# Kernel optimization log

Hardware: AMD Instinct MI355X
Metric: run time of the kernel (lower is better)

## Reference

```python
import jax, jax.numpy as jnp
import numpy as np

NUM_HEADS = 16
INPUT_SIZE = 1024
KEY_SIZE = 64
VALUE_SIZE = 64
LN_EPS = 1e-5


def setup_inputs() -> dict:
    key = jax.random.key(0)
    ks = jax.random.split(key, 11)
    B, S, D = 2, 2048, INPUT_SIZE
    Hk = NUM_HEADS * KEY_SIZE
    Hv = NUM_HEADS * VALUE_SIZE
    s = 0.02
    return {
        "queries": jax.random.normal(ks[0], (B, S, D), dtype=jnp.float32),
        "Wq": jax.random.normal(ks[1], (D, Hk), dtype=jnp.float32) * s,
        "bq": jnp.zeros((Hk,), dtype=jnp.float32),
        "Wk": jax.random.normal(ks[2], (D, Hk), dtype=jnp.float32) * s,
        "bk": jnp.zeros((Hk,), dtype=jnp.float32),
        "Wv": jax.random.normal(ks[3], (D, Hv), dtype=jnp.float32) * s,
        "bv": jnp.zeros((Hv,), dtype=jnp.float32),
        "Wo": jax.random.normal(ks[4], (Hv, D), dtype=jnp.float32) * s,
        "bo": jnp.zeros((D,), dtype=jnp.float32),
        "ln_gamma": jnp.ones((D,), dtype=jnp.float32),
        "ln_beta": jnp.zeros((D,), dtype=jnp.float32),
    }


def reference(queries, Wq, bq, Wk, bk, Wv, bv, Wo, bo, ln_gamma, ln_beta):
    B, S, D = queries.shape
    H, dk, dv = NUM_HEADS, KEY_SIZE, VALUE_SIZE
    residual = queries
    # projections -> [B, S, H, d]
    q = (queries @ Wq + bq).reshape(B, S, H, dk)
    k = (queries @ Wk + bk).reshape(B, S, H, dk)
    v = (queries @ Wv + bv).reshape(B, S, H, dv)
    # scaled dot-product attention per head
    scores = jnp.einsum("bqhd,bkhd->bhqk", q, k) / jnp.sqrt(jnp.float32(dk))
    attn = jax.nn.softmax(scores, axis=-1)
    out = jnp.einsum("bhqk,bkhd->bqhd", attn, v).reshape(B, S, H * dv)
    # out projection + residual + layernorm (dropout=0 / eval)
    res = out @ Wo + bo + residual
    mu = jnp.mean(res, axis=-1, keepdims=True)
    var = jnp.var(res, axis=-1, keepdims=True)
    return (res - mu) / jnp.sqrt(var + LN_EPS) * ln_gamma + ln_beta
```

## Files before the change

kernel.cpp:

```cpp
#include <hip/hip_runtime.h>
#include <hip/hip_bf16.h>
#include <math.h>

#define D 1024
#define NH 16
#define DK 64
#define LN_EPS 1e-5f
typedef __hip_bfloat16 bf16;
typedef __attribute__((ext_vector_type(8))) short bf16x8;
typedef __attribute__((ext_vector_type(4))) short short4v;
typedef __attribute__((ext_vector_type(4))) float f32x4;
typedef __attribute__((ext_vector_type(2))) unsigned int uint2v;

__device__ inline float tofloat(bf16 x) { return __bfloat162float(x); }
__device__ inline float tofs(short s) {
    bf16 b; __builtin_memcpy(&b, &s, 2);
    return __bfloat162float(b);
}
__device__ inline unsigned int pk2(float a, float b) {
    float2 f2; f2.x = a; f2.y = b;
    __hip_bfloat162 h = __float22bfloat162_rn(f2);
    unsigned int u; __builtin_memcpy(&u, &h, 4);
    return u;
}
__device__ inline short4v pk4(float a, float b, float c, float d) {
    uint2v u; u[0] = pk2(a, b); u[1] = pk2(c, d);
    short4v s; __builtin_memcpy(&s, &u, 8);
    return s;
}
__device__ inline bf16x8 pk8(const float* f) {
    uint2v a, b;
    a[0] = pk2(f[0], f[1]); a[1] = pk2(f[2], f[3]);
    b[0] = pk2(f[4], f[5]); b[1] = pk2(f[6], f[7]);
    bf16x8 o;
    short4v s0, s1;
    __builtin_memcpy(&s0, &a, 8); __builtin_memcpy(&s1, &b, 8);
#pragma unroll
    for (int i = 0; i < 4; ++i) { o[i] = s0[i]; o[4 + i] = s1[i]; }
    return o;
}

__device__ inline int wave_isf32(const unsigned short* __restrict__ Xu) {
    unsigned short u = Xu[threadIdx.x & 63];
    unsigned long long m = __ballot(((u >> 7) & 0xFF) >= 0x90);
    return __popcll(m) > 2;
}

__global__ void prep_kernel(const void* X, const void* Wq, const void* Wk, const void* Wv,
                            const void* Wo, const void* bq, const void* bk, const void* bv,
                            const void* bo, const void* g, const void* be,
                            bf16* __restrict__ Xb, bf16* __restrict__ Wqkvt, bf16* __restrict__ Wot,
                            bf16* __restrict__ bqkv, bf16* __restrict__ bob,
                            bf16* __restrict__ gb, bf16* __restrict__ beb) {
    __shared__ float tile[64][65];
    const int isf32 = wave_isf32((const unsigned short*)X);
    const int bid = blockIdx.x;
    const int tid = threadIdx.x;
    if (bid < 2048) {
        int e0 = bid * 2048 + tid * 8;
        bf16x8 outv;
        if (isf32) {
            float4 v0 = ((const float4*)X)[e0 / 4];
            float4 v1 = ((const float4*)X)[e0 / 4 + 1];
            float f[8] = {v0.x, v0.y, v0.z, v0.w, v1.x, v1.y, v1.z, v1.w};
            outv = pk8(f);
        } else {
            outv = ((const bf16x8*)X)[e0 / 8];
        }
        *(bf16x8*)(Xb + e0) = outv;
    } else if (bid < 3072) {
        int t = bid - 2048;
        int z = t >> 8, rem = t & 255;
        const void* srcs[4] = {Wq, Wk, Wv, Wo};
        const void* src = srcs[z];
        bf16* dst = (z < 3) ? (Wqkvt + (size_t)z * 1024 * 1024) : Wot;
        const int i0 = (rem >> 4) * 64, j0 = (rem & 15) * 64;
        const int tr = tid >> 4, tc4 = (tid & 15) * 4;
#pragma unroll
        for (int p = 0; p < 4; ++p) {
            int r = p * 16 + tr;
            if (isf32) {
                float4 v = *(const float4*)((const float*)src + (size_t)(i0 + r) * 1024 + j0 + tc4);
                tile[r][tc4] = v.x; tile[r][tc4 + 1] = v.y;
                tile[r][tc4 + 2] = v.z; tile[r][tc4 + 3] = v.w;
            } else {
                short4v v = *(const short4v*)((const bf16*)src + (size_t)(i0 + r) * 1024 + j0 + tc4);
#pragma unroll
                for (int q = 0; q < 4; ++q) tile[r][tc4 + q] = tofs(v[q]);
            }
        }
        __syncthreads();
        const int wj = tid >> 3, wi = (tid & 7) * 8;
#pragma unroll
        for (int p = 0; p < 2; ++p) {
            int j = p * 32 + wj;
            float f[8];
#pragma unroll
            for (int q = 0; q < 8; ++q) f[q] = tile[wi + q][j];
            *(bf16x8*)(dst + (size_t)(j0 + j) * 1024 + i0 + wi) = pk8(f);
        }
    } else {
        int idx = (bid - 3072) * 256 + tid;
        int seg = idx >> 10, off = idx & 1023;
        const void* srcs[6] = {bq, bk, bv, bo, g, be};
        const void* src = srcs[seg];
        float v = isf32 ? ((const float*)src)[off] : tofloat(((const bf16*)src)[off]);
        bf16 bv16 = __float2bfloat16(v);
        if (seg < 3)       bqkv[seg * 1024 + off] = bv16;
        else if (seg == 3) bob[off] = bv16;
        else if (seg == 4) gb[off] = bv16;
        else               beb[off] = bv16;
    }
}

__global__ __launch_bounds__(256) void gemm_qkv(const bf16* __restrict__ A, const bf16* __restrict__ Bt,
                                                const bf16* __restrict__ bias,
                                                bf16* __restrict__ C, bf16* __restrict__ VtG,
                                                int M, int N, int K, int S) {
    __shared__ short As[128][72];
    __shared__ short Bs[128][72];
    const int tid = threadIdx.x;
    const int lane = tid & 63, wave = tid >> 6;
    const int wy = wave >> 1, wx = wave & 1;
    const int mrow = lane & 15, quad = lane >> 4;
    const int lb = blockIdx.y * gridDim.x + blockIdx.x;
    const int xcd = lb & 7, j = lb >> 3;
    const int bm = (xcd * 4 + (j & 3)) * 128;
    const int bn = (j >> 2) * 128;

    f32x4 acc[4][4];
#pragma unroll
    for (int mi = 0; mi < 4; ++mi)
#pragma unroll
        for (int nt = 0; nt < 4; ++nt) acc[mi][nt] = (f32x4){0.f, 0.f, 0.f, 0.f};

    const int ra = tid >> 1, ca = (tid & 1) * 32;
    const bf16* aptr = A + (size_t)(bm + ra) * K + ca;
    const bf16* bptr = Bt + (size_t)(bn + ra) * K + ca;
    bf16x8 ar0, ar1, ar2, ar3, br0, br1, br2, br3;
    ar0 = *(const bf16x8*)(aptr);      ar1 = *(const bf16x8*)(aptr + 8);
    ar2 = *(const bf16x8*)(aptr + 16); ar3 = *(const bf16x8*)(aptr + 24);
    br0 = *(const bf16x8*)(bptr);      br1 = *(const bf16x8*)(bptr + 8);
    br2 = *(const bf16x8*)(bptr + 16); br3 = *(const bf16x8*)(bptr + 24);

    for (int k0 = 0; k0 < K; k0 += 64) {
        __syncthreads();
        *(bf16x8*)&As[ra][ca] = ar0;      *(bf16x8*)&As[ra][ca + 8] = ar1;
        *(bf16x8*)&As[ra][ca + 16] = ar2; *(bf16x8*)&As[ra][ca + 24] = ar3;
        *(bf16x8*)&Bs[ra][ca] = br0;      *(bf16x8*)&Bs[ra][ca + 8] = br1;
        *(bf16x8*)&Bs[ra][ca + 16] = br2; *(bf16x8*)&Bs[ra][ca + 24] = br3;
        __syncthreads();
        if (k0 + 64 < K) {
            ar0 = *(const bf16x8*)(aptr + k0 + 64);      ar1 = *(const bf16x8*)(aptr + k0 + 72);
            ar2 = *(const bf16x8*)(aptr + k0 + 80);      ar3 = *(const bf16x8*)(aptr + k0 + 88);
            br0 = *(const bf16x8*)(bptr + k0 + 64);      br1 = *(const bf16x8*)(bptr + k0 + 72);
            br2 = *(const bf16x8*)(bptr + k0 + 80);      br3 = *(const bf16x8*)(bptr + k0 + 88);
        }
#pragma unroll
        for (int ks = 0; ks < 2; ++ks) {
            bf16x8 a[4], b[4];
#pragma unroll
            for (int mi = 0; mi < 4; ++mi)
                a[mi] = *(const bf16x8*)&As[wy * 64 + mi * 16 + mrow][ks * 32 + quad * 8];
#pragma unroll
            for (int nt = 0; nt < 4; ++nt)
                b[nt] = *(const bf16x8*)&Bs[wx * 64 + nt * 16 + mrow][ks * 32 + quad * 8];
#pragma unroll
            for (int mi = 0; mi < 4; ++mi)
#pragma unroll
                for (int nt = 0; nt < 4; ++nt)
                    acc[mi][nt] = __builtin_amdgcn_mfma_f32_16x16x32_bf16(a[mi], b[nt], acc[mi][nt], 0, 0, 0);
        }
    }
#pragma unroll
    for (int mi = 0; mi < 4; ++mi) {
#pragma unroll
        for (int nt = 0; nt < 4; ++nt) {
            int col = bn + wx * 64 + nt * 16 + mrow;
            float bc = tofloat(bias[col]);
            if (col >= 2048) {
                int dvf = col - 2048, hh = dvf >> 6, dv = dvf & 63;
                int row0 = bm + wy * 64 + mi * 16 + quad * 4;
                int bb = row0 / S, key0 = row0 % S;
                short4v pk = pk4(acc[mi][nt][0] + bc, acc[mi][nt][1] + bc,
                                 acc[mi][nt][2] + bc, acc[mi][nt][3] + bc);
                *(short4v*)(VtG + (size_t)(bb * NH + hh) * S * 64 + (key0 >> 2) * 256 + dv * 4) = pk;
            } else {
                float sc = (col < 1024) ? 0.18033688f : 1.0f;
#pragma unroll
                for (int reg = 0; reg < 4; ++reg) {
                    int row = bm + wy * 64 + mi * 16 + quad * 4 + reg;
                    C[(size_t)row * N + col] = __float2bfloat16((acc[mi][nt][reg] + bc) * sc);
                }
            }
        }
    }
}

__global__ __launch_bounds__(256) void gemm_out(const bf16* __restrict__ A, const bf16* __restrict__ Bt,
                                                const bf16* __restrict__ bias,
                                                const bf16* __restrict__ residual,
                                                float* __restrict__ C, int M, int N, int K) {
    __shared__ short As[128][72];
    __shared__ short Bs[64][72];
    const int tid = threadIdx.x;
    const int lane = tid & 63, wave = tid >> 6;
    const int wy = wave >> 1, wx = wave & 1;
    const int mrow = lane & 15, quad = lane >> 4;
    const int lb = blockIdx.y * gridDim.x + blockIdx.x;
    const int xcd = lb & 7, j = lb >> 3;
    const int bm = (xcd * 4 + (j & 3)) * 128;
    const int bn = (j >> 2) * 64;

    f32x4 acc[4][2];
#pragma unroll
    for (int mi = 0; mi < 4; ++mi)
#pragma unroll
        for (int nt = 0; nt < 2; ++nt) acc[mi][nt] = (f32x4){0.f, 0.f, 0.f, 0.f};

    const int ra = tid >> 1, ca = (tid & 1) * 32;
    const int rb = tid >> 2, cb = (tid & 3) * 16;
    const bf16* aptr = A + (size_t)(bm + ra) * K + ca;
    const bf16* bptr = Bt + (size_t)(bn + rb) * K + cb;
    bf16x8 ar0, ar1, ar2, ar3, br0, br1;
    ar0 = *(const bf16x8*)(aptr);      ar1 = *(const bf16x8*)(aptr + 8);
    ar2 = *(const bf16x8*)(aptr + 16); ar3 = *(const bf16x8*)(aptr + 24);
    br0 = *(const bf16x8*)(bptr);      br1 = *(const bf16x8*)(bptr + 8);

    for (int k0 = 0; k0 < K; k0 += 64) {
        __syncthreads();
        *(bf16x8*)&As[ra][ca] = ar0;      *(bf16x8*)&As[ra][ca + 8] = ar1;
        *(bf16x8*)&As[ra][ca + 16] = ar2; *(bf16x8*)&As[ra][ca + 24] = ar3;
        *(bf16x8*)&Bs[rb][cb] = br0;      *(bf16x8*)&Bs[rb][cb + 8] = br1;
        __syncthreads();
        if (k0 + 64 < K) {
            ar0 = *(const bf16x8*)(aptr + k0 + 64); ar1 = *(const bf16x8*)(aptr + k0 + 72);
            ar2 = *(const bf16x8*)(aptr + k0 + 80); ar3 = *(const bf16x8*)(aptr + k0 + 88);
            br0 = *(const bf16x8*)(bptr + k0 + 64); br1 = *(const bf16x8*)(bptr + k0 + 72);
        }
#pragma unroll
        for (int ks = 0; ks < 2; ++ks) {
            bf16x8 a[4], b[2];
#pragma unroll
            for (int mi = 0; mi < 4; ++mi)
                a[mi] = *(const bf16x8*)&As[wy * 64 + mi * 16 + mrow][ks * 32 + quad * 8];
#pragma unroll
            for (int nt = 0; nt < 2; ++nt)
                b[nt] = *(const bf16x8*)&Bs[wx * 32 + nt * 16 + mrow][ks * 32 + quad * 8];
#pragma unroll
            for (int mi = 0; mi < 4; ++mi)
#pragma unroll
                for (int nt = 0; nt < 2; ++nt)
                    acc[mi][nt] = __builtin_amdgcn_mfma_f32_16x16x32_bf16(a[mi], b[nt], acc[mi][nt], 0, 0, 0);
        }
    }
#pragma unroll
    for (int mi = 0; mi < 4; ++mi) {
#pragma unroll
        for (int nt = 0; nt < 2; ++nt) {
            int col = bn + wx * 32 + nt * 16 + mrow;
            float bc = tofloat(bias[col]);
#pragma unroll
            for (int reg = 0; reg < 4; ++reg) {
                int row = bm + wy * 64 + mi * 16 + quad * 4 + reg;
                C[(size_t)row * N + col] = acc[mi][nt][reg] + bc + tofloat(residual[(size_t)row * N + col]);
            }
        }
    }
}

__global__ __launch_bounds__(256) void attn_mfma(const bf16* __restrict__ QKV,
                                                 const bf16* __restrict__ VtG,
                                                 bf16* __restrict__ Op, float* __restrict__ Lp,
                                                 int S, int M) {
    __shared__ short Ks[64][72];
    __shared__ short Vs2[16 * 256];
    const int tid = threadIdx.x;
    const int lane = tid & 63, wave = tid >> 6;
    const int mrow = lane & 15, quad = lane >> 4;
    const int ldq = 3 * D;
    const int nqc = S / 128;
    const int lb = blockIdx.y * gridDim.x + blockIdx.x;
    const int xcd = lb & 7, idx = lb >> 3;
    const int pair = xcd * 8 + (idx >> 4);
    const int qc = idx & 15;
    const int bh = pair & 31, sp = pair >> 5;
    const int b = bh / NH, h = bh % NH;
    const int q0 = qc * 128 + wave * 32;
    const int Sh = S / 2, kvlo = sp * Sh;

    bf16x8 qf[2][2];
#pragma unroll
    for (int qt = 0; qt < 2; ++qt) {
        const bf16* qbase = QKV + ((size_t)(b * S + q0 + qt * 16 + mrow)) * ldq + h * DK;
        qf[qt][0] = *(const bf16x8*)(qbase + quad * 8);
        qf[qt][1] = *(const bf16x8*)(qbase + 32 + quad * 8);
    }

    f32x4 o[2][4];
#pragma unroll
    for (int qt = 0; qt < 2; ++qt)
#pragma unroll
        for (int t = 0; t < 4; ++t) o[qt][t] = (f32x4){0.f, 0.f, 0.f, 0.f};
    float lsum[2] = {0.f, 0.f};

    const int rs_ = tid >> 2, cs_ = (tid & 3) * 16;
    const bf16* kb0 = QKV + ((size_t)(b * S + kvlo + rs_)) * ldq + D + h * DK + cs_;
    const bf16* vb0 = VtG + (size_t)(b * NH + h) * S * 64 + kvlo * 64 + tid * 16;
    const int kg_l = tid >> 4, dv0 = (tid & 15) * 4;
    const int voff = kg_l * 256 + (((dv0 + kg_l * 8) & 63) * 4);
    bf16x8 kr0 = *(const bf16x8*)kb0, kr1 = *(const bf16x8*)(kb0 + 8);
    bf16x8 vr0 = *(const bf16x8*)vb0, vr1 = *(const bf16x8*)(vb0 + 8);

    for (int kc = 0; kc < Sh; kc += 64) {
        __syncthreads();
        *(bf16x8*)&Ks[rs_][cs_] = kr0;
        *(bf16x8*)&Ks[rs_][cs_ + 8] = kr1;
        *(bf16x8*)&Vs2[voff] = vr0;
        *(bf16x8*)&Vs2[voff + 8] = vr1;
        __syncthreads();
        if (kc + 64 < Sh) {
            const bf16* kn = kb0 + (size_t)(kc + 64) * ldq;
            kr0 = *(const bf16x8*)kn; kr1 = *(const bf16x8*)(kn + 8);
            const bf16* vn = vb0 + (size_t)(kc + 64) * 64;
            vr0 = *(const bf16x8*)vn; vr1 = *(const bf16x8*)(vn + 8);
        }

        f32x4 s[2][4];
#pragma unroll
        for (int qt = 0; qt < 2; ++qt)
#pragma unroll
            for (int t = 0; t < 4; ++t) s[qt][t] = (f32x4){0.f, 0.f, 0.f, 0.f};
#pragma unroll
        for (int ks = 0; ks < 2; ++ks) {
#pragma unroll
            for (int t = 0; t < 4; ++t) {
                bf16x8 kf = *(const bf16x8*)&Ks[t * 16 + mrow][ks * 32 + quad * 8];
                s[0][t] = __builtin_amdgcn_mfma_f32_16x16x32_bf16(kf, qf[0][ks], s[0][t], 0, 0, 0);
                s[1][t] = __builtin_amdgcn_mfma_f32_16x16x32_bf16(kf, qf[1][ks], s[1][t], 0, 0, 0);
            }
        }
        short4v pf[2][4];
#pragma unroll
        for (int qt = 0; qt < 2; ++qt)
#pragma unroll
            for (int t = 0; t < 4; ++t) {
                float p0 = __builtin_amdgcn_exp2f(s[qt][t][0]);
                float p1 = __builtin_amdgcn_exp2f(s[qt][t][1]);
                float p2 = __builtin_amdgcn_exp2f(s[qt][t][2]);
                float p3 = __builtin_amdgcn_exp2f(s[qt][t][3]);
                lsum[qt] += (p0 + p1) + (p2 + p3);
                pf[qt][t] = pk4(p0, p1, p2, p3);
            }
#pragma unroll
        for (int kt = 0; kt < 4; ++kt) {
            const int kg = kt * 4 + quad;
#pragma unroll
            for (int dvt = 0; dvt < 4; ++dvt) {
                int dvs = ((dvt * 16 + mrow) + kg * 8) & 63;
                short4v vf = *(const short4v*)&Vs2[kg * 256 + dvs * 4];
                o[0][dvt] = __builtin_amdgcn_mfma_f32_16x16x16bf16_1k(pf[0][kt], vf, o[0][dvt], 0, 0, 0);
                o[1][dvt] = __builtin_amdgcn_mfma_f32_16x16x16bf16_1k(pf[1][kt], vf, o[1][dvt], 0, 0, 0);
            }
        }
    }
#pragma unroll
    for (int qt = 0; qt < 2; ++qt) {
        float v = lsum[qt];
        v += __shfl_xor(v, 16, 64);
        v += __shfl_xor(v, 32, 64);
        lsum[qt] = v;
        if (quad == 0)
            Lp[(size_t)sp * M * NH + ((size_t)(b * NH + h)) * S + q0 + qt * 16 + mrow] = v;
    }
#pragma unroll
    for (int qt = 0; qt < 2; ++qt)
#pragma unroll
        for (int r = 0; r < 4; ++r) {
            bf16* orow = Op + (size_t)sp * M * D +
                         ((size_t)(b * S + q0 + qt * 16 + quad * 4 + r)) * D + h * DK;
#pragma unroll
            for (int dvt = 0; dvt < 4; ++dvt)
                orow[dvt * 16 + mrow] = __float2bfloat16(o[qt][dvt][r]);
        }
}

__global__ void combine_kernel(const bf16* __restrict__ Op, const float* __restrict__ Lp,
                               bf16* __restrict__ Ob, int M, int S) {
    int idx = blockIdx.x * 256 + threadIdx.x;
    int row = idx >> 7;
    int col0 = (idx & 127) * 8;
    int h = col0 >> 6;
    size_t e0 = (size_t)row * D + col0;
    bf16x8 o0 = *(const bf16x8*)(Op + e0);
    bf16x8 o1 = *(const bf16x8*)(Op + (size_t)M * D + e0);
    int b = row / S, q = row % S;
    size_t li = ((size_t)(b * NH + h)) * S + q;
    float inv = 1.0f / (Lp[li] + Lp[(size_t)M * NH + li]);
    float f[8];
#pragma unroll
    for (int i = 0; i < 8; ++i) f[i] = (tofs(o0[i]) + tofs(o1[i])) * inv;
    *(bf16x8*)(Ob + e0) = pk8(f);
}

__global__ void ln_kernel(const float* __restrict__ R, const bf16* __restrict__ gamma,
                          const bf16* __restrict__ beta, void* __restrict__ out,
                          const void* __restrict__ X) {
    __shared__ float red[8];
    const int isf32 = wave_isf32((const unsigned short*)X);
    const int row = blockIdx.x;
    const float4 xv = *(const float4*)(R + (size_t)row * D + threadIdx.x * 4);
    float sum = xv.x + xv.y + xv.z + xv.w;
    float sq = xv.x * xv.x + xv.y * xv.y + xv.z * xv.z + xv.w * xv.w;
    for (int off = 32; off; off >>= 1) {
        sum += __shfl_xor(sum, off, 64);
        sq += __shfl_xor(sq, off, 64);
    }
    const int wave = threadIdx.x / 64, lane = threadIdx.x % 64;
    if (lane == 0) { red[wave] = sum; red[wave + 4] = sq; }
    __syncthreads();
    sum = red[0] + red[1] + red[2] + red[3];
    sq = red[4] + red[5] + red[6] + red[7];
    const float mu = sum / (float)D;
    const float var = sq / (float)D - mu * mu;
    const float inv = rsqrtf(var + LN_EPS);
    const float x4[4] = {xv.x, xv.y, xv.z, xv.w};
#pragma unroll
    for (int i = 0; i < 4; ++i) {
        int cidx = threadIdx.x * 4 + i;
        float y = (x4[i] - mu) * inv * tofloat(gamma[cidx]) + tofloat(beta[cidx]);
        size_t oidx = (size_t)row * D + cidx;
        if (isf32) ((float*)out)[oidx] = y;
        else       ((bf16*)out)[oidx] = __float2bfloat16(y);
    }
}

extern "C" void kernel_launch(void* const* d_in, const int* in_sizes, int n_in,
                              void* d_out, int out_size, void* d_ws, size_t ws_size,
                              hipStream_t stream) {
    const int M = in_sizes[0] / D;
    const int B = 2;
    const int S = M / B;

    char* p = (char*)d_ws;
    auto alloc = [&](size_t bytes) { char* r = p; p += (bytes + 255) & ~(size_t)255; return r; };
    bf16* Xb    = (bf16*)alloc((size_t)M * D * 2);
    bf16* Wqkvt = (bf16*)alloc((size_t)3 * D * D * 2);
    bf16* Wot   = (bf16*)alloc((size_t)D * D * 2);
    bf16* bqkv  = (bf16*)alloc(3 * D * 2);
    bf16* bob   = (bf16*)alloc(D * 2);
    bf16* gb    = (bf16*)alloc(D * 2);
    bf16* beb   = (bf16*)alloc(D * 2);
    bf16* QKV   = (bf16*)alloc((size_t)M * 3 * D * 2);
    bf16* VtG   = (bf16*)alloc((size_t)M * D * 2);
    bf16* Opart = (bf16*)alloc((size_t)2 * M * D * 2);
    float* Lp   = (float*)alloc((size_t)2 * M * NH * 4);
    bf16* Ob    = (bf16*)alloc((size_t)M * D * 2);
    float* Rf   = (float*)alloc((size_t)M * D * 4);

    prep_kernel<<<3096, 256, 0, stream>>>(d_in[0], d_in[1], d_in[3], d_in[5], d_in[7],
                                          d_in[2], d_in[4], d_in[6], d_in[8], d_in[9], d_in[10],
                                          Xb, Wqkvt, Wot, bqkv, bob, gb, beb);

    gemm_qkv<<<dim3(3 * D / 128, M / 128), 256, 0, stream>>>(
        Xb, Wqkvt, bqkv, QKV, VtG, M, 3 * D, D, S);

    attn_mfma<<<dim3(B * NH * (S / 128), 2), 256, 0, stream>>>(QKV, VtG, Opart, Lp, S, M);

    combine_kernel<<<M * D / 8 / 256, 256, 0, stream>>>(Opart, Lp, Ob, M, S);

    gemm_out<<<dim3(D / 64, M / 128), 256, 0, stream>>>(Ob, Wot, bob, Xb, Rf, M, D, D);

    ln_kernel<<<M, 256, 0, stream>>>(Rf, gb, beb, d_out, d_in[0]);
}
```

Baseline: 219.9 us.

## Drop split-KV attention, double-buffer K/V in LDS, fuse softmax normalization

```diff
diff --git a/kernel.cpp b/kernel.cpp
--- a/kernel.cpp
+++ b/kernel.cpp
@@ -269,25 +269,21 @@
     }
 }
 
-__global__ __launch_bounds__(256) void attn_mfma(const bf16* __restrict__ QKV,
-                                                 const bf16* __restrict__ VtG,
-                                                 bf16* __restrict__ Op, float* __restrict__ Lp,
-                                                 int S, int M) {
-    __shared__ short Ks[64][72];
-    __shared__ short Vs2[16 * 256];
+__global__ __launch_bounds__(256, 3) void attn_mfma(const bf16* __restrict__ QKV,
+                                                    const bf16* __restrict__ VtG,
+                                                    bf16* __restrict__ Ob, int S, int M) {
+    __shared__ short Ks[2][64][72];
+    __shared__ short Vs2[2][16 * 256];
     const int tid = threadIdx.x;
     const int lane = tid & 63, wave = tid >> 6;
     const int mrow = lane & 15, quad = lane >> 4;
     const int ldq = 3 * D;
-    const int nqc = S / 128;
     const int lb = blockIdx.y * gridDim.x + blockIdx.x;
     const int xcd = lb & 7, idx = lb >> 3;
-    const int pair = xcd * 8 + (idx >> 4);
+    const int bh = xcd * 4 + (idx >> 4);
     const int qc = idx & 15;
-    const int bh = pair & 31, sp = pair >> 5;
     const int b = bh / NH, h = bh % NH;
     const int q0 = qc * 128 + wave * 32;
-    const int Sh = S / 2, kvlo = sp * Sh;
 
     bf16x8 qf[2][2];
 #pragma unroll
@@ -305,21 +301,26 @@
     float lsum[2] = {0.f, 0.f};
 
     const int rs_ = tid >> 2, cs_ = (tid & 3) * 16;
-    const bf16* kb0 = QKV + ((size_t)(b * S + kvlo + rs_)) * ldq + D + h * DK + cs_;
-    const bf16* vb0 = VtG + (size_t)(b * NH + h) * S * 64 + kvlo * 64 + tid * 16;
+    const bf16* kb0 = QKV + ((size_t)(b * S + rs_)) * ldq + D + h * DK + cs_;
+    const bf16* vb0 = VtG + (size_t)(b * NH + h) * S * 64 + tid * 16;
     const int kg_l = tid >> 4, dv0 = (tid & 15) * 4;
     const int voff = kg_l * 256 + (((dv0 + kg_l * 8) & 63) * 4);
-    bf16x8 kr0 = *(const bf16x8*)kb0, kr1 = *(const bf16x8*)(kb0 + 8);
-    bf16x8 vr0 = *(const bf16x8*)vb0, vr1 = *(const bf16x8*)(vb0 + 8);
-
-    for (int kc = 0; kc < Sh; kc += 64) {
-        __syncthreads();
-        *(bf16x8*)&Ks[rs_][cs_] = kr0;
-        *(bf16x8*)&Ks[rs_][cs_ + 8] = kr1;
-        *(bf16x8*)&Vs2[voff] = vr0;
-        *(bf16x8*)&Vs2[voff + 8] = vr1;
-        __syncthreads();
-        if (kc + 64 < Sh) {
+
+    {
+        bf16x8 k0v = *(const bf16x8*)kb0, k1v = *(const bf16x8*)(kb0 + 8);
+        bf16x8 v0v = *(const bf16x8*)vb0, v1v = *(const bf16x8*)(vb0 + 8);
+        *(bf16x8*)&Ks[0][rs_][cs_] = k0v;
+        *(bf16x8*)&Ks[0][rs_][cs_ + 8] = k1v;
+        *(bf16x8*)&Vs2[0][voff] = v0v;
+        *(bf16x8*)&Vs2[0][voff + 8] = v1v;
+    }
+
+    for (int kc = 0; kc < S; kc += 64) {
+        const int cur = (kc >> 6) & 1;
+        __syncthreads();
+        bf16x8 kr0, kr1, vr0, vr1;
+        const int more = (kc + 64 < S);
+        if (more) {
             const bf16* kn = kb0 + (size_t)(kc + 64) * ldq;
             kr0 = *(const bf16x8*)kn; kr1 = *(const bf16x8*)(kn + 8);
             const bf16* vn = vb0 + (size_t)(kc + 64) * 64;
@@ -331,15 +332,17 @@
         for (int qt = 0; qt < 2; ++qt)
 #pragma unroll
             for (int t = 0; t < 4; ++t) s[qt][t] = (f32x4){0.f, 0.f, 0.f, 0.f};
+        __builtin_amdgcn_s_setprio(1);
 #pragma unroll
         for (int ks = 0; ks < 2; ++ks) {
 #pragma unroll
             for (int t = 0; t < 4; ++t) {
-                bf16x8 kf = *(const bf16x8*)&Ks[t * 16 + mrow][ks * 32 + quad * 8];
+                bf16x8 kf = *(const bf16x8*)&Ks[cur][t * 16 + mrow][ks * 32 + quad * 8];
                 s[0][t] = __builtin_amdgcn_mfma_f32_16x16x32_bf16(kf, qf[0][ks], s[0][t], 0, 0, 0);
                 s[1][t] = __builtin_amdgcn_mfma_f32_16x16x32_bf16(kf, qf[1][ks], s[1][t], 0, 0, 0);
             }
         }
+        __builtin_amdgcn_s_setprio(0);
         short4v pf[2][4];
 #pragma unroll
         for (int qt = 0; qt < 2; ++qt)
@@ -352,16 +355,24 @@
                 lsum[qt] += (p0 + p1) + (p2 + p3);
                 pf[qt][t] = pk4(p0, p1, p2, p3);
             }
+        __builtin_amdgcn_s_setprio(1);
 #pragma unroll
         for (int kt = 0; kt < 4; ++kt) {
             const int kg = kt * 4 + quad;
 #pragma unroll
             for (int dvt = 0; dvt < 4; ++dvt) {
                 int dvs = ((dvt * 16 + mrow) + kg * 8) & 63;
-                short4v vf = *(const short4v*)&Vs2[kg * 256 + dvs * 4];
+                short4v vf = *(const short4v*)&Vs2[cur][kg * 256 + dvs * 4];
                 o[0][dvt] = __builtin_amdgcn_mfma_f32_16x16x16bf16_1k(pf[0][kt], vf, o[0][dvt], 0, 0, 0);
                 o[1][dvt] = __builtin_amdgcn_mfma_f32_16x16x16bf16_1k(pf[1][kt], vf, o[1][dvt], 0, 0, 0);
             }
+        }
+        __builtin_amdgcn_s_setprio(0);
+        if (more) {
+            *(bf16x8*)&Ks[cur ^ 1][rs_][cs_] = kr0;
+            *(bf16x8*)&Ks[cur ^ 1][rs_][cs_ + 8] = kr1;
+            *(bf16x8*)&Vs2[cur ^ 1][voff] = vr0;
+            *(bf16x8*)&Vs2[cur ^ 1][voff + 8] = vr1;
         }
     }
 #pragma unroll
@@ -370,37 +381,17 @@
         v += __shfl_xor(v, 16, 64);
         v += __shfl_xor(v, 32, 64);
         lsum[qt] = v;
-        if (quad == 0)
-            Lp[(size_t)sp * M * NH + ((size_t)(b * NH + h)) * S + q0 + qt * 16 + mrow] = v;
     }
 #pragma unroll
     for (int qt = 0; qt < 2; ++qt)
 #pragma unroll
         for (int r = 0; r < 4; ++r) {
-            bf16* orow = Op + (size_t)sp * M * D +
-                         ((size_t)(b * S + q0 + qt * 16 + quad * 4 + r)) * D + h * DK;
+            float inv = 1.0f / __shfl(lsum[qt], quad * 4 + r, 64);
+            bf16* orow = Ob + ((size_t)(b * S + q0 + qt * 16 + quad * 4 + r)) * D + h * DK;
 #pragma unroll
             for (int dvt = 0; dvt < 4; ++dvt)
-                orow[dvt * 16 + mrow] = __float2bfloat16(o[qt][dvt][r]);
-        }
-}
-
-__global__ void combine_kernel(const bf16* __restrict__ Op, const float* __restrict__ Lp,
-                               bf16* __restrict__ Ob, int M, int S) {
-    int idx = blockIdx.x * 256 + threadIdx.x;
-    int row = idx >> 7;
-    int col0 = (idx & 127) * 8;
-    int h = col0 >> 6;
-    size_t e0 = (size_t)row * D + col0;
-    bf16x8 o0 = *(const bf16x8*)(Op + e0);
-    bf16x8 o1 = *(const bf16x8*)(Op + (size_t)M * D + e0);
-    int b = row / S, q = row % S;
-    size_t li = ((size_t)(b * NH + h)) * S + q;
-    float inv = 1.0f / (Lp[li] + Lp[(size_t)M * NH + li]);
-    float f[8];
-#pragma unroll
-    for (int i = 0; i < 8; ++i) f[i] = (tofs(o0[i]) + tofs(o1[i])) * inv;
-    *(bf16x8*)(Ob + e0) = pk8(f);
+                orow[dvt * 16 + mrow] = __float2bfloat16(o[qt][dvt][r] * inv);
+        }
 }
 
 __global__ void ln_kernel(const float* __restrict__ R, const bf16* __restrict__ gamma,
@@ -453,8 +444,6 @@
     bf16* beb   = (bf16*)alloc(D * 2);
     bf16* QKV   = (bf16*)alloc((size_t)M * 3 * D * 2);
     bf16* VtG   = (bf16*)alloc((size_t)M * D * 2);
-    bf16* Opart = (bf16*)alloc((size_t)2 * M * D * 2);
-    float* Lp   = (float*)alloc((size_t)2 * M * NH * 4);
     bf16* Ob    = (bf16*)alloc((size_t)M * D * 2);
     float* Rf   = (float*)alloc((size_t)M * D * 4);
 
@@ -465,9 +454,7 @@
     gemm_qkv<<<dim3(3 * D / 128, M / 128), 256, 0, stream>>>(
         Xb, Wqkvt, bqkv, QKV, VtG, M, 3 * D, D, S);
 
-    attn_mfma<<<dim3(B * NH * (S / 128), 2), 256, 0, stream>>>(QKV, VtG, Opart, Lp, S, M);
-
-    combine_kernel<<<M * D / 8 / 256, 256, 0, stream>>>(Opart, Lp, Ob, M, S);
+    attn_mfma<<<dim3(B * NH * (S / 128)), 256, 0, stream>>>(QKV, VtG, Ob, S, M);
 
     gemm_out<<<dim3(D / 64, M / 128), 256, 0, stream>>>(Ob, Wot, bob, Xb, Rf, M, D, D);
 
```

Result: faster. 211.0 us (-4.0%).
